# Kernel optimization log

Hardware: AMD Instinct MI355X
Metric: run time of the kernel (lower is better)

Reference implementation:

```python
import jax, jax.numpy as jnp
import numpy as np

OUT_SIZE = 7          # pooled output resolution
SR = 2                # sampling_ratio (samples per bin side)
SCALES = (0.25, 0.125, 0.0625, 0.03125)   # FPN P2..P5 -> min_level=2, max_level=5
MIN_LEVEL, MAX_LEVEL = 2, 5
CANON_SIZE, CANON_LEVEL = 224.0, 4.0


def _roi_align(feat, boxes, bidx, scale):
    """ROIAlignV2 (aligned=True), fixed sampling_ratio.
    feat: [N,C,H,W]; boxes: [M,4] (x1,y1,x2,y2 in image coords); bidx: [M] int.
    Returns [M,C,OUT_SIZE,OUT_SIZE]."""
    N, C, H, W = feat.shape
    featT = jnp.transpose(feat, (0, 2, 3, 1))  # [N,H,W,C] for channel-last gathers
    # aligned=True: half-pixel offset
    x1 = boxes[:, 0] * scale - 0.5
    y1 = boxes[:, 1] * scale - 0.5
    x2 = boxes[:, 2] * scale - 0.5
    y2 = boxes[:, 3] * scale - 0.5
    bw = (x2 - x1) / OUT_SIZE
    bh = (y2 - y1) / OUT_SIZE
    # flattened per-bin sample offsets: for bin i, sample j -> i + (j+0.5)/SR
    k = jnp.arange(OUT_SIZE * SR)
    off = (k // SR).astype(feat.dtype) + ((k % SR).astype(feat.dtype) + 0.5) / SR  # [P]
    ys = y1[:, None] + off[None, :] * bh[:, None]  # [M,P]
    xs = x1[:, None] + off[None, :] * bw[:, None]  # [M,P]
    # validity (torchvision semantics: zero outside [-1, size])
    vy = (ys >= -1.0) & (ys <= H)
    vx = (xs >= -1.0) & (xs <= W)
    valid = vy[:, :, None] & vx[:, None, :]        # [M,P,P]
    y = jnp.clip(ys, 0.0, H - 1.0)
    x = jnp.clip(xs, 0.0, W - 1.0)
    y0 = jnp.floor(y).astype(jnp.int32)
    x0 = jnp.floor(x).astype(jnp.int32)
    y1i = jnp.minimum(y0 + 1, H - 1)
    x1i = jnp.minimum(x0 + 1, W - 1)
    ly = y - y0.astype(y.dtype)
    lx = x - x0.astype(x.dtype)
    hy, hx = 1.0 - ly, 1.0 - lx

    def gather(yi, xi):  # -> [M,P,P,C]
        return featT[bidx[:, None, None], yi[:, :, None], xi[:, None, :]]

    val = (hy[:, :, None] * hx[:, None, :])[..., None] * gather(y0, x0)
    val = val + (hy[:, :, None] * lx[:, None, :])[..., None] * gather(y0, x1i)
    val = val + (ly[:, :, None] * hx[:, None, :])[..., None] * gather(y1i, x0)
    val = val + (ly[:, :, None] * lx[:, None, :])[..., None] * gather(y1i, x1i)
    val = jnp.where(valid[..., None], val, 0.0)
    M = boxes.shape[0]
    # average SRxSR samples per bin
    val = val.reshape(M, OUT_SIZE, SR, OUT_SIZE, SR, C).mean(axis=(2, 4))
    return jnp.transpose(val, (0, 3, 1, 2))  # [M,C,7,7]


def _pool(feats, boxes):
    N, R, _ = boxes.shape
    b = boxes.reshape(-1, 4)                        # [M,4], M = N*R (pooler-format concat)
    bidx = jnp.repeat(jnp.arange(N), R)             # batch index column
    # assign_boxes_to_levels: log2 area bucketing
    sizes = jnp.sqrt(jnp.maximum((b[:, 2] - b[:, 0]) * (b[:, 3] - b[:, 1]), 0.0))
    lvl = jnp.floor(CANON_LEVEL + jnp.log2(sizes / CANON_SIZE + 1e-8))
    lvl = jnp.clip(lvl, MIN_LEVEL, MAX_LEVEL).astype(jnp.int32) - MIN_LEVEL  # [M] in [0,3]
    out = jnp.zeros((b.shape[0], feats[0].shape[1], OUT_SIZE, OUT_SIZE), feats[0].dtype)
    for l, (f, s) in enumerate(zip(feats, SCALES)):
        pooled = _roi_align(f, b, bidx, s)
        out = out + jnp.where((lvl == l)[:, None, None, None], pooled, 0.0)
    return out


def setup_inputs() -> dict:
    key = jax.random.key(0)
    ks = jax.random.split(key, 6)
    N, R, IMG = 2, 512, 1024.0
    shapes = [(2, 256, 256, 256), (2, 256, 128, 128), (2, 256, 64, 64), (2, 256, 32, 32)]
    feats = [jax.random.normal(ks[i], s, dtype=jnp.float32) for i, s in enumerate(shapes)]
    # box sizes log-uniform in [32, 800] px so all 4 levels get boxes
    wh = jnp.exp(jax.random.uniform(ks[4], (N, R, 2), minval=jnp.log(32.0), maxval=jnp.log(800.0)))
    cxy = jax.random.uniform(ks[5], (N, R, 2), minval=0.0, maxval=IMG)
    x1y1 = jnp.clip(cxy - wh / 2, 0.0, IMG)
    x2y2 = jnp.clip(cxy + wh / 2, 0.0, IMG)
    boxes = jnp.concatenate([x1y1, x2y2], axis=-1)  # [N,R,4]
    return {"feat0": feats[0], "feat1": feats[1], "feat2": feats[2], "feat3": feats[3], "boxes": boxes}


def reference(feat0, feat1, feat2, feat3, boxes):
    return _pool((feat0, feat1, feat2, feat3), boxes)
```

## Files before the change

### kernel.cpp

```cpp
#include <hip/hip_runtime.h>

#define OUT 7
#define CCH 256

__device__ __forceinline__ unsigned short f2bf(float f) {
    union { float f; unsigned int u; } v; v.f = f;
    unsigned int r = (v.u + 0x7FFFu + ((v.u >> 16) & 1u)) >> 16;
    return (unsigned short)r;
}
__device__ __forceinline__ float bf2f(unsigned short h) {
    union { unsigned int u; float f; } v; v.u = ((unsigned int)h) << 16;
    return v.f;
}
__device__ __forceinline__ float bf2f_lo(unsigned int u) {
    union { unsigned int u; float f; } v; v.u = u << 16;
    return v.f;
}
__device__ __forceinline__ float bf2f_hi(unsigned int u) {
    union { unsigned int u; float f; } v; v.u = u & 0xFFFF0000u;
    return v.f;
}

__global__ __launch_bounds__(256) void roi_pool_naive(
    const float* __restrict__ f0, const float* __restrict__ f1,
    const float* __restrict__ f2, const float* __restrict__ f3,
    const float* __restrict__ boxes, float* __restrict__ out,
    int M, int R)
{
    int idx = blockIdx.x * blockDim.x + threadIdx.x;
    int total = M * CCH * OUT * OUT;
    if (idx >= total) return;
    int pw = idx % OUT;
    int ph = (idx / OUT) % OUT;
    int c  = (idx / (OUT * OUT)) % CCH;
    int m  = idx / (OUT * OUT * CCH);
    int n  = m / R;
    const float bx1 = boxes[m * 4 + 0], by1 = boxes[m * 4 + 1];
    const float bx2 = boxes[m * 4 + 2], by2 = boxes[m * 4 + 3];
    float sz  = sqrtf(fmaxf((bx2 - bx1) * (by2 - by1), 0.0f));
    int lvl = (int)floorf(4.0f + log2f(sz / 224.0f + 1e-8f));
    lvl = min(max(lvl, 2), 5) - 2;
    const float* feat; int H, W; float scale;
    switch (lvl) {
        case 0:  feat = f0; H = 256; W = 256; scale = 0.25f;    break;
        case 1:  feat = f1; H = 128; W = 128; scale = 0.125f;   break;
        case 2:  feat = f2; H = 64;  W = 64;  scale = 0.0625f;  break;
        default: feat = f3; H = 32;  W = 32;  scale = 0.03125f; break;
    }
    const float* fp = feat + (size_t)(n * CCH + c) * (size_t)(H * W);
    float x1 = bx1 * scale - 0.5f, y1 = by1 * scale - 0.5f;
    float x2 = bx2 * scale - 0.5f, y2 = by2 * scale - 0.5f;
    float bw = (x2 - x1) * (1.0f / OUT), bh = (y2 - y1) * (1.0f / OUT);
    float acc = 0.0f;
    #pragma unroll
    for (int iy = 0; iy < 2; iy++) {
        float ys = y1 + ((float)ph + ((float)iy + 0.5f) * 0.5f) * bh;
        bool vy = (ys >= -1.0f) && (ys <= (float)H);
        float y = fminf(fmaxf(ys, 0.0f), (float)(H - 1));
        int y0 = (int)y;
        int y1i = min(y0 + 1, H - 1);
        float ly = y - (float)y0, hy = 1.0f - ly;
        #pragma unroll
        for (int ix = 0; ix < 2; ix++) {
            float xs = x1 + ((float)pw + ((float)ix + 0.5f) * 0.5f) * bw;
            bool vx = (xs >= -1.0f) && (xs <= (float)W);
            float x = fminf(fmaxf(xs, 0.0f), (float)(W - 1));
            int x0 = (int)x;
            int x1ii = min(x0 + 1, W - 1);
            float lx = x - (float)x0, hx = 1.0f - lx;
            if (vy && vx) {
                acc += hy * hx * fp[y0 * W + x0]  + hy * lx * fp[y0 * W + x1ii]
                     + ly * hx * fp[y1i * W + x0] + ly * lx * fp[y1i * W + x1ii];
            }
        }
    }
    out[idx] = acc * 0.25f;
}

__global__ __launch_bounds__(256) void transpose_all(
    const float* __restrict__ f0, const float* __restrict__ f1,
    const float* __restrict__ f2, const float* __restrict__ f3,
    unsigned short* __restrict__ o0, unsigned short* __restrict__ o1,
    unsigned short* __restrict__ o2, unsigned short* __restrict__ o3,
    int N)
{
    __shared__ float tile[64][65];

    int rem = blockIdx.x;
    const int nb0 = 4096 * N;
    const int nb1 = 1024 * N;
    const int nb2 = 256 * N;
    const float* in; unsigned short* op; int HW, lshift;
    if (rem < nb0)        { in = f0; op = o0; HW = 65536; lshift = 10; }
    else { rem -= nb0;
      if (rem < nb1)      { in = f1; op = o1; HW = 16384; lshift = 8;  }
      else { rem -= nb1;
        if (rem < nb2)    { in = f2; op = o2; HW = 4096;  lshift = 6;  }
        else { rem -= nb2;  in = f3; op = o3; HW = 1024;  lshift = 4;  }
      }
    }
    int hw0 = (rem & ((1 << lshift) - 1)) << 6;
    int c0  = ((rem >> lshift) & 3) << 6;
    int n   = rem >> (lshift + 2);

    int tid = threadIdx.x;
    int tx = tid & 15;
    int ty = tid >> 4;

    const float4* in4 = (const float4*)(in + (size_t)n * CCH * HW);
    #pragma unroll
    for (int j = 0; j < 4; j++) {
        int c = c0 + ty + 16 * j;
        float4 v = in4[((size_t)c * HW + hw0) / 4 + tx];
        tile[ty + 16 * j][4 * tx + 0] = v.x;
        tile[ty + 16 * j][4 * tx + 1] = v.y;
        tile[ty + 16 * j][4 * tx + 2] = v.z;
        tile[ty + 16 * j][4 * tx + 3] = v.w;
    }
    __syncthreads();
    unsigned short* ob = op + (size_t)n * HW * CCH;
    #pragma unroll
    for (int j = 0; j < 4; j++) {
        int hw = hw0 + ty + 16 * j;
        ushort4 u;
        u.x = f2bf(tile[4 * tx + 0][ty + 16 * j]);
        u.y = f2bf(tile[4 * tx + 1][ty + 16 * j]);
        u.z = f2bf(tile[4 * tx + 2][ty + 16 * j]);
        u.w = f2bf(tile[4 * tx + 3][ty + 16 * j]);
        ((ushort4*)(ob + (size_t)hw * CCH + c0))[tx] = u;
    }
}

__global__ __launch_bounds__(128) void roi_pool_cl2(
    const unsigned short* __restrict__ t0, const unsigned short* __restrict__ t1,
    const unsigned short* __restrict__ t2, const unsigned short* __restrict__ t3,
    const float* __restrict__ boxes, float* __restrict__ out, int M, int R)
{
    int bx = blockIdx.x;
    int m, ph;
    if ((M & 7) == 0) {
        int q = bx / 56, rem = bx - q * 56;
        ph = rem >> 3;
        m  = q * 8 + (rem & 7);
    } else {
        m = bx / OUT; ph = bx % OUT;
    }
    int t = threadIdx.x;
    int n = m / R;

    const float bx1 = boxes[m * 4 + 0], by1 = boxes[m * 4 + 1];
    const float bx2 = boxes[m * 4 + 2], by2 = boxes[m * 4 + 3];
    float sz  = sqrtf(fmaxf((bx2 - bx1) * (by2 - by1), 0.0f));
    int lvl = (int)floorf(4.0f + log2f(sz / 224.0f + 1e-8f));
    lvl = min(max(lvl, 2), 5) - 2;

    const unsigned short* feat; int H, W; float scale;
    switch (lvl) {
        case 0:  feat = t0; H = 256; W = 256; scale = 0.25f;    break;
        case 1:  feat = t1; H = 128; W = 128; scale = 0.125f;   break;
        case 2:  feat = t2; H = 64;  W = 64;  scale = 0.0625f;  break;
        default: feat = t3; H = 32;  W = 32;  scale = 0.03125f; break;
    }
    const unsigned short* fb = feat + (size_t)n * H * W * CCH;

    float x1 = bx1 * scale - 0.5f, y1 = by1 * scale - 0.5f;
    float x2 = bx2 * scale - 0.5f, y2 = by2 * scale - 0.5f;
    float bw = (x2 - x1) * (1.0f / OUT), bh = (y2 - y1) * (1.0f / OUT);

    int   r0[2], r1[2];
    float lyv[2], hyv[2];
    bool  vyv[2];
    #pragma unroll
    for (int iy = 0; iy < 2; iy++) {
        float ys = y1 + ((float)ph + ((float)iy + 0.5f) * 0.5f) * bh;
        vyv[iy] = (ys >= -1.0f) && (ys <= (float)H);
        float y = fminf(fmaxf(ys, 0.0f), (float)(H - 1));
        int y0 = (int)y;
        int y1i = min(y0 + 1, H - 1);
        lyv[iy] = y - (float)y0;
        hyv[iy] = 1.0f - lyv[iy];
        r0[iy] = y0 * W * CCH;
        r1[iy] = y1i * W * CCH;
    }

    float accA[OUT];
    float accB[OUT];
    #pragma unroll
    for (int pw = 0; pw < OUT; pw++) {
        float aA = 0.0f, aB = 0.0f;
        #pragma unroll
        for (int ix = 0; ix < 2; ix++) {
            float xs = x1 + ((float)pw + ((float)ix + 0.5f) * 0.5f) * bw;
            bool vx = (xs >= -1.0f) && (xs <= (float)W);
            float x = fminf(fmaxf(xs, 0.0f), (float)(W - 1));
            int x0 = (int)x;
            int x1i = min(x0 + 1, W - 1);
            float lx = x - (float)x0;
            float hx = 1.0f - lx;
            int c0o = x0 * CCH;
            int c1o = x1i * CCH;
            #pragma unroll
            for (int iy = 0; iy < 2; iy++) {
                if (vyv[iy] && vx) {
                    const unsigned int* p00 = (const unsigned int*)(fb + __builtin_amdgcn_readfirstlane(r0[iy] + c0o));
                    const unsigned int* p01 = (const unsigned int*)(fb + __builtin_amdgcn_readfirstlane(r0[iy] + c1o));
                    const unsigned int* p10 = (const unsigned int*)(fb + __builtin_amdgcn_readfirstlane(r1[iy] + c0o));
                    const unsigned int* p11 = (const unsigned int*)(fb + __builtin_amdgcn_readfirstlane(r1[iy] + c1o));
                    unsigned int u00 = p00[t], u01 = p01[t];
                    unsigned int u10 = p10[t], u11 = p11[t];
                    float w00 = hyv[iy] * hx, w01 = hyv[iy] * lx;
                    float w10 = lyv[iy] * hx, w11 = lyv[iy] * lx;
                    aA += w00 * bf2f_lo(u00) + w01 * bf2f_lo(u01)
                        + w10 * bf2f_lo(u10) + w11 * bf2f_lo(u11);
                    aB += w00 * bf2f_hi(u00) + w01 * bf2f_hi(u01)
                        + w10 * bf2f_hi(u10) + w11 * bf2f_hi(u11);
                }
            }
        }
        accA[pw] = aA * 0.25f;
        accB[pw] = aB * 0.25f;
    }

    float* obA = out + (size_t)m * (CCH * OUT * OUT) + (size_t)(2 * t) * (OUT * OUT) + ph * OUT;
    float* obB = obA + (OUT * OUT);
    #pragma unroll
    for (int k = 0; k < OUT; k++) obA[k] = accA[k];
    #pragma unroll
    for (int k = 0; k < OUT; k++) obB[k] = accB[k];
}

extern "C" void kernel_launch(void* const* d_in, const int* in_sizes, int n_in,
                              void* d_out, int out_size, void* d_ws, size_t ws_size,
                              hipStream_t stream) {
    const float* f0    = (const float*)d_in[0];
    const float* f1    = (const float*)d_in[1];
    const float* f2    = (const float*)d_in[2];
    const float* f3    = (const float*)d_in[3];
    const float* boxes = (const float*)d_in[4];
    float* out = (float*)d_out;

    int N = in_sizes[0] / (CCH * 256 * 256);
    int M = in_sizes[4] / 4;
    int R = M / N;

    size_t nshorts = (size_t)N * CCH * (65536 + 16384 + 4096 + 1024);
    if (ws_size >= nshorts * sizeof(unsigned short)) {
        unsigned short* t0 = (unsigned short*)d_ws;
        unsigned short* t1 = t0 + (size_t)N * CCH * 65536;
        unsigned short* t2 = t1 + (size_t)N * CCH * 16384;
        unsigned short* t3 = t2 + (size_t)N * CCH * 4096;
        int tblocks = (4096 + 1024 + 256 + 64) * N;
        transpose_all<<<tblocks, 256, 0, stream>>>(f0, f1, f2, f3, t0, t1, t2, t3, N);
        roi_pool_cl2<<<M * OUT, 128, 0, stream>>>(t0, t1, t2, t3, boxes, out, M, R);
    } else {
        int total = M * CCH * OUT * OUT;
        roi_pool_naive<<<(total + 255) / 256, 256, 0, stream>>>(f0, f1, f2, f3, boxes, out, M, R);
    }
}
```

Measured before the change: 296.6 us.

## Transpose full channel depth per block with bf16-packed swizzled LDS tile

The NCHW-to-NHWC bf16 transpose now has each block cover all 256 channels for a 64-pixel strip instead of a 64x64 channel/pixel tile. Values are converted to bf16 and packed in pairs before going into a swizzled LDS buffer, which halves LDS footprint and traffic. Each output pixel row is then written as full 512-byte contiguous uint4 stores. This targets store coalescing and LDS bank conflicts in the transpose, which reads the whole feature pyramid. The cost is 4x fewer blocks, more work per thread, and extra shift/mask work to unpack halves.

Result: no change. 296.1 us (-0.1%).

```diff
diff --git a/kernel.cpp b/kernel.cpp
--- a/kernel.cpp
+++ b/kernel.cpp
@@ -7,10 +7,6 @@
     union { float f; unsigned int u; } v; v.f = f;
     unsigned int r = (v.u + 0x7FFFu + ((v.u >> 16) & 1u)) >> 16;
     return (unsigned short)r;
-}
-__device__ __forceinline__ float bf2f(unsigned short h) {
-    union { unsigned int u; float f; } v; v.u = ((unsigned int)h) << 16;
-    return v.f;
 }
 __device__ __forceinline__ float bf2f_lo(unsigned int u) {
     union { unsigned int u; float f; } v; v.u = u << 16;
@@ -84,12 +80,12 @@
     unsigned short* __restrict__ o2, unsigned short* __restrict__ o3,
     int N)
 {
-    __shared__ float tile[64][65];
+    __shared__ unsigned int lds[CCH][32];
 
     int rem = blockIdx.x;
-    const int nb0 = 4096 * N;
-    const int nb1 = 1024 * N;
-    const int nb2 = 256 * N;
+    const int nb0 = 1024 * N;
+    const int nb1 = 256 * N;
+    const int nb2 = 64 * N;
     const float* in; unsigned short* op; int HW, lshift;
     if (rem < nb0)        { in = f0; op = o0; HW = 65536; lshift = 10; }
     else { rem -= nb0;
@@ -100,34 +96,46 @@
       }
     }
     int hw0 = (rem & ((1 << lshift) - 1)) << 6;
-    int c0  = ((rem >> lshift) & 3) << 6;
-    int n   = rem >> (lshift + 2);
-
-    int tid = threadIdx.x;
-    int tx = tid & 15;
-    int ty = tid >> 4;
+    int n   = rem >> lshift;
+
+    int t  = threadIdx.x;
+    int tx = t & 15;
+    int ty = t >> 4;
 
     const float4* in4 = (const float4*)(in + (size_t)n * CCH * HW);
     #pragma unroll
-    for (int j = 0; j < 4; j++) {
-        int c = c0 + ty + 16 * j;
-        float4 v = in4[((size_t)c * HW + hw0) / 4 + tx];
-        tile[ty + 16 * j][4 * tx + 0] = v.x;
-        tile[ty + 16 * j][4 * tx + 1] = v.y;
-        tile[ty + 16 * j][4 * tx + 2] = v.z;
-        tile[ty + 16 * j][4 * tx + 3] = v.w;
+    for (int j = 0; j < 16; j++) {
+        int c = ty + 16 * j;
+        float4 v = in4[((size_t)c * HW + (size_t)hw0) / 4 + tx];
+        unsigned int u0 = (unsigned int)f2bf(v.x) | ((unsigned int)f2bf(v.y) << 16);
+        unsigned int u1 = (unsigned int)f2bf(v.z) | ((unsigned int)f2bf(v.w) << 16);
+        int e   = 2 * (c >> 3) + 8 * (c & 3);
+        int col = (2 * tx + e) & 31;
+        *(uint2*)(&lds[c][col]) = make_uint2(u0, u1);
     }
     __syncthreads();
+
+    int txc  = t & 31;
+    int row8 = t >> 5;
     unsigned short* ob = op + (size_t)n * HW * CCH;
     #pragma unroll
-    for (int j = 0; j < 4; j++) {
-        int hw = hw0 + ty + 16 * j;
-        ushort4 u;
-        u.x = f2bf(tile[4 * tx + 0][ty + 16 * j]);
-        u.y = f2bf(tile[4 * tx + 1][ty + 16 * j]);
-        u.z = f2bf(tile[4 * tx + 2][ty + 16 * j]);
-        u.w = f2bf(tile[4 * tx + 3][ty + 16 * j]);
-        ((ushort4*)(ob + (size_t)hw * CCH + c0))[tx] = u;
+    for (int p = 0; p < 8; p++) {
+        int hwl = 8 * p + row8;
+        int hwp = hwl >> 1;
+        int sel = hwl & 1;
+        unsigned int w[4];
+        #pragma unroll
+        for (int kk = 0; kk < 4; kk++) {
+            int ca = 8 * txc + 2 * kk;
+            int cb = ca + 1;
+            unsigned int ua = lds[ca][(hwp + 2 * txc + 8 * ((2 * kk) & 3)) & 31];
+            unsigned int ub = lds[cb][(hwp + 2 * txc + 8 * ((2 * kk + 1) & 3)) & 31];
+            unsigned int ha = sel ? (ua >> 16)          : (ua & 0xFFFFu);
+            unsigned int hb = sel ? (ub & 0xFFFF0000u)  : (ub << 16);
+            w[kk] = ha | hb;
+        }
+        uint4 vv; vv.x = w[0]; vv.y = w[1]; vv.z = w[2]; vv.w = w[3];
+        ((uint4*)(ob + (size_t)(hw0 + hwl) * CCH))[txc] = vv;
     }
 }
 
@@ -249,7 +257,7 @@
         unsigned short* t1 = t0 + (size_t)N * CCH * 65536;
         unsigned short* t2 = t1 + (size_t)N * CCH * 16384;
         unsigned short* t3 = t2 + (size_t)N * CCH * 4096;
-        int tblocks = (4096 + 1024 + 256 + 64) * N;
+        int tblocks = (1024 + 256 + 64 + 16) * N;
         transpose_all<<<tblocks, 256, 0, stream>>>(f0, f1, f2, f3, t0, t1, t2, t3, N);
         roi_pool_cl2<<<M * OUT, 128, 0, stream>>>(t0, t1, t2, t3, boxes, out, M, R);
     } else {
```
